# Optimization experiments

Hardware: AMD Instinct MI355X
Metric: run time of the kernel (lower is better)

Reference implementation:

```python
import jax, jax.numpy as jnp
import numpy as np

R_ITER = 3
EPS = 1e-7  # keras.backend.epsilon()


def squash(v, axis=-1):
    s2 = jnp.sum(jnp.square(v), axis=axis, keepdims=True)
    scale = s2 / (1.0 + s2) / jnp.sqrt(s2 + EPS)
    return scale * v


def setup_inputs() -> dict:
    key = jax.random.key(0)
    kx, kw = jax.random.split(key)
    B, N_IN, D_IN = 64, 2048, 8
    N_OUT, D_OUT = 32, 16
    x = jax.random.normal(kx, (B, N_IN, D_IN), dtype=jnp.float32)
    # W matches keras weight (1, N_IN//shared, N_OUT, D_OUT, D_IN) with shared=1,
    # stored here without the leading broadcast dim. RandomNormal(stddev=0.1).
    W = 0.1 * jax.random.normal(kw, (N_IN, N_OUT, D_OUT, D_IN), dtype=jnp.float32)
    return {"x": x, "W": W}


def reference(x, W):
    # predictions u_hat[b, i, j, :] = W[i, j] @ x[b, i]  -> [B, N_in, N_out, D_out]
    preds = jnp.einsum('nodi,bni->bnod', W, x)
    N_in, N_out = preds.shape[1], preds.shape[2]
    # raw routing logits start at zeros with broadcast batch dim (as in TF code)
    raw = jnp.zeros((1, N_in, N_out), dtype=x.dtype)
    for i in range(R_ITER):
        rw = jax.nn.softmax(raw, axis=2)                      # softmax over output caps
        s = jnp.sum(rw[..., None] * preds, axis=1)            # [B, N_out, D_out]
        v = squash(s, axis=-1)                                # squash over capsule dim
        if i < R_ITER - 1:
            # agreement: <u_hat_ij, v_j>
            raw = raw + jnp.einsum('bnod,bod->bno', preds, v)
    return v, rw
```

## Files before the change

### kernel.cpp

```cpp
#include <hip/hip_runtime.h>

static constexpr int B_    = 64;
static constexpr int N_    = 2048;
static constexpr int DI_   = 8;
static constexpr int O_    = 32;
static constexpr int P_    = 16;
static constexpr int OP_   = O_ * P_;
static constexpr int M_    = OP_ * B_;
static constexpr int CHUNK_ = 8;
static constexpr int NBLK_  = N_ / CHUNK_;
static constexpr int WSLICE_ = O_ * P_ * DI_;

template <int CTRL>
__device__ __forceinline__ float dpp_add(float v) {
  int t = __builtin_amdgcn_update_dpp(0, __float_as_int(v), CTRL, 0xf, 0xf, false);
  return v + __int_as_float(t);
}

__device__ __forceinline__ float rfl(float v) {
  return __int_as_float(__builtin_amdgcn_readfirstlane(__float_as_int(v)));
}

template <int MODE, bool ATOMIC>
__global__ __launch_bounds__(1024, 4)
void fused_pass(const float* __restrict__ x, const float* __restrict__ W,
                const float* __restrict__ v_in, float* __restrict__ s_out,
                float* __restrict__ rw_out) {
  __shared__ __align__(16) float w_lds[WSLICE_];
  const int tid  = threadIdx.x;
  const int lane = tid & 63;
  const int wave = tid >> 6;
  const int wu   = __builtin_amdgcn_readfirstlane(wave);
  const int o    = lane >> 1;
  const int ph   = lane & 1;
  const int n0   = blockIdx.x * CHUNK_;

  const int swoff = (tid ^ ((tid >> 4) & 7)) * 4;
  const int wbase = lane * 64 + (lane & 7) * 4;

  float vv[4][8];
  if (MODE != 0) {
    #pragma unroll
    for (int bb = 0; bb < 4; ++bb) {
      const float4* vp = (const float4*)(v_in + (size_t)(wu * 4 + bb) * OP_ +
                                         o * P_ + ph * 8);
      const float4 a = vp[0], c = vp[1];
      vv[bb][0] = a.x; vv[bb][1] = a.y; vv[bb][2] = a.z; vv[bb][3] = a.w;
      vv[bb][4] = c.x; vv[bb][5] = c.y; vv[bb][6] = c.z; vv[bb][7] = c.w;
    }
  }

  float s_r[4][8];
  #pragma unroll
  for (int bb = 0; bb < 4; ++bb)
    #pragma unroll
    for (int pp = 0; pp < 8; ++pp) s_r[bb][pp] = 0.0f;

  {
    const float4 w0 = *(const float4*)(W + (size_t)n0 * WSLICE_ + tid * 4);
    *(float4*)&w_lds[swoff] = w0;
  }
  __syncthreads();

  #pragma unroll 1
  for (int nn = 0; nn < CHUNK_; ++nn) {
    const int n = n0 + nn;

    float4 wreg;
    if (nn + 1 < CHUNK_)
      wreg = *(const float4*)(W + (size_t)(n + 1) * WSLICE_ + tid * 4);

    float xs[4][8];
    #pragma unroll
    for (int bb = 0; bb < 4; ++bb) {
      const float* xp = x + (size_t)(wu * 4 + bb) * (N_ * DI_) + (size_t)n * DI_;
      const float4 xa = *(const float4*)xp;
      const float4 xc = *(const float4*)(xp + 4);
      xs[bb][0] = rfl(xa.x); xs[bb][1] = rfl(xa.y);
      xs[bb][2] = rfl(xa.z); xs[bb][3] = rfl(xa.w);
      xs[bb][4] = rfl(xc.x); xs[bb][5] = rfl(xc.y);
      xs[bb][6] = rfl(xc.z); xs[bb][7] = rfl(xc.w);
    }

    float pr[4][8];
    float acc[4] = {0.0f, 0.0f, 0.0f, 0.0f};

    #pragma unroll
    for (int pp = 0; pp < 8; ++pp) {
      const float4 w0 = *(const float4*)&w_lds[wbase ^ (8 * pp)];
      const float4 w1 = *(const float4*)&w_lds[wbase ^ (8 * pp + 4)];
      #pragma unroll
      for (int bb = 0; bb < 4; ++bb) {
        float pv = w0.x * xs[bb][0];
        pv = __builtin_fmaf(w0.y, xs[bb][1], pv);
        pv = __builtin_fmaf(w0.z, xs[bb][2], pv);
        pv = __builtin_fmaf(w0.w, xs[bb][3], pv);
        pv = __builtin_fmaf(w1.x, xs[bb][4], pv);
        pv = __builtin_fmaf(w1.y, xs[bb][5], pv);
        pv = __builtin_fmaf(w1.z, xs[bb][6], pv);
        pv = __builtin_fmaf(w1.w, xs[bb][7], pv);
        if (MODE == 0) {
          s_r[bb][pp] += pv;
        } else {
          pr[bb][pp] = pv;
          acc[bb] = __builtin_fmaf(pv, vv[bb][pp], acc[bb]);
        }
      }
    }

    if (MODE != 0) {
      #pragma unroll
      for (int bb = 0; bb < 4; ++bb) {
        const float full = dpp_add<0xB1>(acc[bb]);
        const float e = __expf(full);
        float srow = e;
        srow = dpp_add<0x121>(srow);
        srow = dpp_add<0x122>(srow);
        srow = dpp_add<0x124>(srow);
        srow = dpp_add<0x128>(srow);
        float t2 = srow + __shfl_xor(srow, 16);
        const float S = t2 + __shfl_xor(t2, 32);
        const float rw = (2.0f * e) / S;
        #pragma unroll
        for (int pp = 0; pp < 8; ++pp)
          s_r[bb][pp] = __builtin_fmaf(rw, pr[bb][pp], s_r[bb][pp]);
        if (MODE == 2) {
          if (ph == 0)
            rw_out[((size_t)(wu * 4 + bb) * N_ + n) * O_ + o] = rw;
        }
      }
    }

    if (nn + 1 < CHUNK_) {
      __syncthreads();
      *(float4*)&w_lds[swoff] = wreg;
      __syncthreads();
    }
  }

  if (ATOMIC) {
    #pragma unroll
    for (int bb = 0; bb < 4; ++bb) {
      #pragma unroll
      for (int h = 0; h < 2; ++h)
        #pragma unroll
        for (int j = 0; j < 4; ++j)
          atomicAdd(&s_out[(size_t)(wu * 4 + bb) * 512 + h * 256 + lane * 4 + j],
                    s_r[bb][h * 4 + j]);
    }
  } else {
    #pragma unroll
    for (int bb = 0; bb < 4; ++bb) {
      float* sp = s_out + (size_t)blockIdx.x * M_ + (size_t)(wu * 4 + bb) * 512 +
                  lane * 4;
      float4 st0, st1;
      st0.x = s_r[bb][0]; st0.y = s_r[bb][1]; st0.z = s_r[bb][2]; st0.w = s_r[bb][3];
      st1.x = s_r[bb][4]; st1.y = s_r[bb][5]; st1.z = s_r[bb][6]; st1.w = s_r[bb][7];
      *(float4*)sp = st0;
      *(float4*)(sp + 256) = st1;
    }
  }
}

__global__ __launch_bounds__(1024)
void reduce1(const float* __restrict__ spart, float* __restrict__ p2, int K) {
  const int g  = blockIdx.x >> 4;
  const int mc = blockIdx.x & 15;
  const int kpg = K >> 4;
  const int m0 = mc * 2048 + threadIdx.x;
  float a0 = 0.0f, a1 = 0.0f;
  const float* p = spart + (size_t)(g * kpg) * M_;
  for (int k = 0; k < kpg; ++k) {
    a0 += p[(size_t)k * M_ + m0];
    a1 += p[(size_t)k * M_ + m0 + 1024];
  }
  p2[(size_t)g * M_ + m0]        = a0;
  p2[(size_t)g * M_ + m0 + 1024] = a1;
}

__global__ __launch_bounds__(1024)
void v_kernel(const float* __restrict__ src, int ngroups, float scale,
              const float* __restrict__ v_add, float* __restrict__ v_out,
              float* __restrict__ zero_buf) {
  __shared__ float sq[P_ * 65];
  const int t = threadIdx.x;
  const int p = t & 15;
  const int b = t >> 4;
  const int o = blockIdx.x;
  const int q = o * P_ + p;
  const int idx_src = b * 512 + ((p >> 2) & 1) * 256 + (2 * o + (p >> 3)) * 4 +
                      (p & 3);
  float acc = 0.0f;
  for (int g = 0; g < ngroups; ++g)
    acc += src[(size_t)g * M_ + idx_src];
  acc *= scale;
  sq[p * 65 + b] = acc * acc;
  if (zero_buf) zero_buf[blockIdx.x * 1024 + t] = 0.0f;
  __syncthreads();
  float s2 = 0.0f;
  #pragma unroll
  for (int pp = 0; pp < P_; ++pp) s2 += sq[pp * 65 + b];
  float sc = (s2 / (1.0f + s2)) / sqrtf(s2 + 1e-7f);
  float v = acc * sc;
  const int idx = b * OP_ + q;
  v_out[idx] = v + (v_add ? v_add[idx] : 0.0f);
}

extern "C" void kernel_launch(void* const* d_in, const int* in_sizes, int n_in,
                              void* d_out, int out_size, void* d_ws, size_t ws_size,
                              hipStream_t stream) {
  (void)in_sizes; (void)n_in; (void)out_size;
  const float* x = (const float*)d_in[0];
  const float* W = (const float*)d_in[1];
  float* out_v  = (float*)d_out;
  float* out_rw = out_v + (size_t)B_ * O_ * P_;
  float* vws   = (float*)d_ws;
  float* vsum  = vws + M_;
  float* p2    = vsum + M_;
  float* spart = p2 + 16 * M_;

  const size_t need = (size_t)(2 * M_ + 16 * M_ + (size_t)NBLK_ * M_) * 4;

  dim3 gF(NBLK_), bF(1024), gV(O_), bV(1024), gR(256);
  if (ws_size >= need) {
    fused_pass<0, false><<<gF, bF, 0, stream>>>(x, W, nullptr, spart, nullptr);
    reduce1<<<gR, bF, 0, stream>>>(spart, p2, NBLK_);
    v_kernel<<<gV, bV, 0, stream>>>(p2, 16, 1.0f / 32.0f, nullptr, vws, nullptr);
    fused_pass<1, false><<<gF, bF, 0, stream>>>(x, W, vws, spart, nullptr);
    reduce1<<<gR, bF, 0, stream>>>(spart, p2, NBLK_);
    v_kernel<<<gV, bV, 0, stream>>>(p2, 16, 1.0f, vws, vsum, nullptr);
    fused_pass<2, false><<<gF, bF, 0, stream>>>(x, W, vsum, spart, out_rw);
    reduce1<<<gR, bF, 0, stream>>>(spart, p2, NBLK_);
    v_kernel<<<gV, bV, 0, stream>>>(p2, 16, 1.0f, nullptr, out_v, nullptr);
  } else {
    float* sAb = p2;
    float* sBb = sAb + M_;
    hipMemsetAsync(sAb, 0, (size_t)M_ * sizeof(float), stream);
    fused_pass<0, true><<<gF, bF, 0, stream>>>(x, W, nullptr, sAb, nullptr);
    v_kernel<<<gV, bV, 0, stream>>>(sAb, 1, 1.0f / 32.0f, nullptr, vws, sBb);
    fused_pass<1, true><<<gF, bF, 0, stream>>>(x, W, vws, sBb, nullptr);
    v_kernel<<<gV, bV, 0, stream>>>(sBb, 1, 1.0f, vws, vsum, sAb);
    fused_pass<2, true><<<gF, bF, 0, stream>>>(x, W, vsum, sAb, out_rw);
    v_kernel<<<gV, bV, 0, stream>>>(sAb, 1, 1.0f, nullptr, out_v, nullptr);
  }
}
```

Measured before the change: 271.9 us.

## Split fused pass blocks across batch halves and load routing vectors lazily

Each fused-pass block now covers half the batch with 512 threads, so twice as many blocks process the same input chunk, and each thread loads two W float4s into LDS. The v vectors are no longer held in registers for the whole loop; they are reloaded per batch element and the agreement dot product is computed after the predictions. This aims to cut register pressure and raise parallelism, but each W slice is now read from global memory by two blocks and v is re-fetched on every iteration.

```diff
diff --git a/kernel.cpp b/kernel.cpp
--- a/kernel.cpp
+++ b/kernel.cpp
@@ -22,33 +22,25 @@
 }
 
 template <int MODE, bool ATOMIC>
-__global__ __launch_bounds__(1024, 4)
+__global__ __launch_bounds__(512, 2)
 void fused_pass(const float* __restrict__ x, const float* __restrict__ W,
                 const float* __restrict__ v_in, float* __restrict__ s_out,
                 float* __restrict__ rw_out) {
   __shared__ __align__(16) float w_lds[WSLICE_];
   const int tid  = threadIdx.x;
   const int lane = tid & 63;
-  const int wave = tid >> 6;
-  const int wu   = __builtin_amdgcn_readfirstlane(wave);
+  const int wu   = __builtin_amdgcn_readfirstlane(tid >> 6);
   const int o    = lane >> 1;
   const int ph   = lane & 1;
-  const int n0   = blockIdx.x * CHUNK_;
-
-  const int swoff = (tid ^ ((tid >> 4) & 7)) * 4;
+  const int cn   = blockIdx.x >> 1;
+  const int bh   = blockIdx.x & 1;
+  const int n0   = cn * CHUNK_;
+  const int b0   = bh * 32 + wu * 4;
+
+  const int t2  = tid + 512;
+  const int sw0 = (tid ^ ((tid >> 4) & 7)) * 4;
+  const int sw1 = (t2  ^ ((t2  >> 4) & 7)) * 4;
   const int wbase = lane * 64 + (lane & 7) * 4;
-
-  float vv[4][8];
-  if (MODE != 0) {
-    #pragma unroll
-    for (int bb = 0; bb < 4; ++bb) {
-      const float4* vp = (const float4*)(v_in + (size_t)(wu * 4 + bb) * OP_ +
-                                         o * P_ + ph * 8);
-      const float4 a = vp[0], c = vp[1];
-      vv[bb][0] = a.x; vv[bb][1] = a.y; vv[bb][2] = a.z; vv[bb][3] = a.w;
-      vv[bb][4] = c.x; vv[bb][5] = c.y; vv[bb][6] = c.z; vv[bb][7] = c.w;
-    }
-  }
 
   float s_r[4][8];
   #pragma unroll
@@ -57,8 +49,10 @@
     for (int pp = 0; pp < 8; ++pp) s_r[bb][pp] = 0.0f;
 
   {
-    const float4 w0 = *(const float4*)(W + (size_t)n0 * WSLICE_ + tid * 4);
-    *(float4*)&w_lds[swoff] = w0;
+    const float4 a = *(const float4*)(W + (size_t)n0 * WSLICE_ + tid * 4);
+    const float4 b = *(const float4*)(W + (size_t)n0 * WSLICE_ + t2 * 4);
+    *(float4*)&w_lds[sw0] = a;
+    *(float4*)&w_lds[sw1] = b;
   }
   __syncthreads();
 
@@ -66,14 +60,16 @@
   for (int nn = 0; nn < CHUNK_; ++nn) {
     const int n = n0 + nn;
 
-    float4 wreg;
-    if (nn + 1 < CHUNK_)
-      wreg = *(const float4*)(W + (size_t)(n + 1) * WSLICE_ + tid * 4);
+    float4 wrA, wrB;
+    if (nn + 1 < CHUNK_) {
+      wrA = *(const float4*)(W + (size_t)(n + 1) * WSLICE_ + tid * 4);
+      wrB = *(const float4*)(W + (size_t)(n + 1) * WSLICE_ + t2 * 4);
+    }
 
     float xs[4][8];
     #pragma unroll
     for (int bb = 0; bb < 4; ++bb) {
-      const float* xp = x + (size_t)(wu * 4 + bb) * (N_ * DI_) + (size_t)n * DI_;
+      const float* xp = x + (size_t)(b0 + bb) * (N_ * DI_) + (size_t)n * DI_;
       const float4 xa = *(const float4*)xp;
       const float4 xc = *(const float4*)(xp + 4);
       xs[bb][0] = rfl(xa.x); xs[bb][1] = rfl(xa.y);
@@ -83,8 +79,6 @@
     }
 
     float pr[4][8];
-    float acc[4] = {0.0f, 0.0f, 0.0f, 0.0f};
-
     #pragma unroll
     for (int pp = 0; pp < 8; ++pp) {
       const float4 w0 = *(const float4*)&w_lds[wbase ^ (8 * pp)];
@@ -99,41 +93,50 @@
         pv = __builtin_fmaf(w1.y, xs[bb][5], pv);
         pv = __builtin_fmaf(w1.z, xs[bb][6], pv);
         pv = __builtin_fmaf(w1.w, xs[bb][7], pv);
-        if (MODE == 0) {
-          s_r[bb][pp] += pv;
-        } else {
-          pr[bb][pp] = pv;
-          acc[bb] = __builtin_fmaf(pv, vv[bb][pp], acc[bb]);
-        }
+        if (MODE == 0) s_r[bb][pp] += pv;
+        else           pr[bb][pp] = pv;
       }
     }
 
     if (MODE != 0) {
       #pragma unroll
       for (int bb = 0; bb < 4; ++bb) {
-        const float full = dpp_add<0xB1>(acc[bb]);
+        const float4* vp = (const float4*)(v_in + (size_t)(b0 + bb) * OP_ +
+                                           o * P_ + ph * 8);
+        const float4 va = vp[0];
+        const float4 vc = vp[1];
+        float acc = pr[bb][0] * va.x;
+        acc = __builtin_fmaf(pr[bb][1], va.y, acc);
+        acc = __builtin_fmaf(pr[bb][2], va.z, acc);
+        acc = __builtin_fmaf(pr[bb][3], va.w, acc);
+        acc = __builtin_fmaf(pr[bb][4], vc.x, acc);
+        acc = __builtin_fmaf(pr[bb][5], vc.y, acc);
+        acc = __builtin_fmaf(pr[bb][6], vc.z, acc);
+        acc = __builtin_fmaf(pr[bb][7], vc.w, acc);
+        const float full = dpp_add<0xB1>(acc);
         const float e = __expf(full);
         float srow = e;
         srow = dpp_add<0x121>(srow);
         srow = dpp_add<0x122>(srow);
         srow = dpp_add<0x124>(srow);
         srow = dpp_add<0x128>(srow);
-        float t2 = srow + __shfl_xor(srow, 16);
-        const float S = t2 + __shfl_xor(t2, 32);
+        float t16 = srow + __shfl_xor(srow, 16);
+        const float S = t16 + __shfl_xor(t16, 32);
         const float rw = (2.0f * e) / S;
         #pragma unroll
         for (int pp = 0; pp < 8; ++pp)
           s_r[bb][pp] = __builtin_fmaf(rw, pr[bb][pp], s_r[bb][pp]);
         if (MODE == 2) {
           if (ph == 0)
-            rw_out[((size_t)(wu * 4 + bb) * N_ + n) * O_ + o] = rw;
+            rw_out[((size_t)(b0 + bb) * N_ + n) * O_ + o] = rw;
         }
       }
     }
 
     if (nn + 1 < CHUNK_) {
       __syncthreads();
-      *(float4*)&w_lds[swoff] = wreg;
+      *(float4*)&w_lds[sw0] = wrA;
+      *(float4*)&w_lds[sw1] = wrB;
       __syncthreads();
     }
   }
@@ -145,14 +148,13 @@
       for (int h = 0; h < 2; ++h)
         #pragma unroll
         for (int j = 0; j < 4; ++j)
-          atomicAdd(&s_out[(size_t)(wu * 4 + bb) * 512 + h * 256 + lane * 4 + j],
+          atomicAdd(&s_out[(size_t)(b0 + bb) * 512 + h * 256 + lane * 4 + j],
                     s_r[bb][h * 4 + j]);
     }
   } else {
     #pragma unroll
     for (int bb = 0; bb < 4; ++bb) {
-      float* sp = s_out + (size_t)blockIdx.x * M_ + (size_t)(wu * 4 + bb) * 512 +
-                  lane * 4;
+      float* sp = s_out + (size_t)cn * M_ + (size_t)(b0 + bb) * 512 + lane * 4;
       float4 st0, st1;
       st0.x = s_r[bb][0]; st0.y = s_r[bb][1]; st0.z = s_r[bb][2]; st0.w = s_r[bb][3];
       st1.x = s_r[bb][4]; st1.y = s_r[bb][5]; st1.z = s_r[bb][6]; st1.w = s_r[bb][7];
@@ -221,16 +223,16 @@
 
   const size_t need = (size_t)(2 * M_ + 16 * M_ + (size_t)NBLK_ * M_) * 4;
 
-  dim3 gF(NBLK_), bF(1024), gV(O_), bV(1024), gR(256);
+  dim3 gF(2 * NBLK_), bF(512), gV(O_), bV(1024), gR(256), bR(1024);
   if (ws_size >= need) {
     fused_pass<0, false><<<gF, bF, 0, stream>>>(x, W, nullptr, spart, nullptr);
-    reduce1<<<gR, bF, 0, stream>>>(spart, p2, NBLK_);
+    reduce1<<<gR, bR, 0, stream>>>(spart, p2, NBLK_);
     v_kernel<<<gV, bV, 0, stream>>>(p2, 16, 1.0f / 32.0f, nullptr, vws, nullptr);
     fused_pass<1, false><<<gF, bF, 0, stream>>>(x, W, vws, spart, nullptr);
-    reduce1<<<gR, bF, 0, stream>>>(spart, p2, NBLK_);
+    reduce1<<<gR, bR, 0, stream>>>(spart, p2, NBLK_);
     v_kernel<<<gV, bV, 0, stream>>>(p2, 16, 1.0f, vws, vsum, nullptr);
     fused_pass<2, false><<<gF, bF, 0, stream>>>(x, W, vsum, spart, out_rw);
-    reduce1<<<gR, bF, 0, stream>>>(spart, p2, NBLK_);
+    reduce1<<<gR, bR, 0, stream>>>(spart, p2, NBLK_);
     v_kernel<<<gV, bV, 0, stream>>>(p2, 16, 1.0f, nullptr, out_v, nullptr);
   } else {
     float* sAb = p2;
```

After: 224.6 us. -17.4%, faster.
